# Optimization experiments

Hardware: AMD Instinct MI355X
Metric: run time of the kernel (lower is better)

The kernel has to match this reference:

```python
import jax, jax.numpy as jnp
import numpy as np
from jax import lax

SPATIAL_K = 30
FEATURE_K = 6
EPS = 1e-12  # F.normalize eps


def setup_inputs() -> dict:
    key = jax.random.key(0)
    k1, k2 = jax.random.split(key)
    N, D = 10000, 256
    ema_feat = jax.random.normal(k1, (N, D), dtype=jnp.float32)
    pos = jax.random.randint(k2, (N, 2), 0, 512, dtype=jnp.int64)
    return {"ema_feat": ema_feat, "pos": pos}


def _spatial_candidates(pos, k_spatial):
    # Brute-force k-NN on 2D integer positions (replaces sklearn KD-tree).
    posf = pos.astype(jnp.float32)  # [N, 2]
    sq = jnp.sum(posf * posf, axis=-1)  # [N]
    d2 = sq[:, None] + sq[None, :] - 2.0 * (posf @ posf.T)  # [N, N]
    N = pos.shape[0]
    # exclude self (sklearn returns self first, code drops column 0)
    d2 = d2 + jnp.where(jnp.eye(N, dtype=bool), jnp.inf, 0.0).astype(d2.dtype)
    _, idx = lax.top_k(-d2, k_spatial)  # nearest = largest negative distance
    return idx  # [N, k_spatial]


def reference(ema_feat, pos):
    N = ema_feat.shape[0]
    k_spatial = min(SPATIAL_K, N - 1)
    k_feat = min(FEATURE_K, k_spatial)

    spatial_candidates = _spatial_candidates(pos, k_spatial)  # [N, Ks]

    # F.normalize(ema_feat, dim=-1): x / max(||x||, eps)
    norm = jnp.linalg.norm(ema_feat, axis=-1, keepdims=True)
    feat_norm = ema_feat / jnp.maximum(norm, EPS)  # [N, D]

    cand_feat = feat_norm[spatial_candidates]  # [N, Ks, D]
    sim = jnp.einsum("nd,nkd->nk", feat_norm, cand_feat)  # cosine sim [N, Ks]

    topk_sim, topk_local_idx = lax.top_k(sim, k_feat)  # [N, Kf]
    topk_indices = jnp.take_along_axis(spatial_candidates, topk_local_idx, axis=1)
    topk_weights = jax.nn.softmax(topk_sim, axis=-1)
    return topk_indices, topk_weights
```

## Files before the change

### kernel.cpp

```cpp
#include <hip/hip_runtime.h>
#include <cstdint>
#include <cstddef>

#define FD    256
#define KS    30
#define KF    6
#define CSH   4
#define GW    32
#define NCELLS (GW*GW)
#define BCAP  40
#define OVCAP 128
#define KREG  8
#define SCAPW 96
#define MAXC  100
#define PIPE  5

#define WFENCE() __threadfence_block()

__global__ __launch_bounds__(1024) void zero_kernel(int* __restrict__ cellCnt,
                                                    int* __restrict__ ovfCnt) {
  cellCnt[threadIdx.x] = 0;
  if (threadIdx.x == 0) *ovfCnt = 0;
}

__global__ __launch_bounds__(256) void prep_bin_kernel(const float* __restrict__ x,
                                                       float* __restrict__ y,
                                                       const int2* __restrict__ pos,
                                                       int* __restrict__ cellCnt,
                                                       int2* __restrict__ bucket,
                                                       int* __restrict__ ovfCnt,
                                                       int2* __restrict__ ovf, int N) {
  const int j = blockIdx.x * 256 + threadIdx.x;
  if (j < N) {
    int2 p = pos[j];
    const int cell = (p.y >> CSH) * GW + (p.x >> CSH);
    const int s = atomicAdd(&cellCnt[cell], 1);
    const int2 e = make_int2(p.x | (p.y << 16), j);
    if (s < BCAP) bucket[cell * BCAP + s] = e;
    else { int o = atomicAdd(ovfCnt, 1); if (o < OVCAP) ovf[o] = e; }
  }
  const int row = blockIdx.x * 4 + (threadIdx.x >> 6);
  if (row >= N) return;
  const int lane = threadIdx.x & 63;
  float4 v = ((const float4*)(x + (size_t)row * FD))[lane];
  float ss = v.x * v.x + v.y * v.y + v.z * v.z + v.w * v.w;
#pragma unroll
  for (int o = 32; o; o >>= 1) ss += __shfl_down(ss, o);
  ss = __shfl(ss, 0);
  const float d = fmaxf(sqrtf(ss), 1e-12f);
  float4 o4;
  o4.x = v.x / d; o4.y = v.y / d; o4.z = v.z / d; o4.w = v.w / d;
  ((float4*)(y + (size_t)row * FD))[lane] = o4;
}

__global__ __launch_bounds__(256) void compact_kernel(const int* __restrict__ cellCnt,
                                                      const int2* __restrict__ bucket,
                                                      const int* __restrict__ ovfCnt,
                                                      const int2* __restrict__ ovf,
                                                      int* __restrict__ qorder, int N) {
  const int w = threadIdx.x >> 6, lane = threadIdx.x & 63;
  const int cell = blockIdx.x * 4 + w;
  const int4* cc4 = (const int4*)cellCnt;
  int start = 0, total = 0;
#pragma unroll
  for (int c = 0; c < 4; ++c) {
    int4 v = cc4[c * 64 + lane];
    int s0 = min(v.x, BCAP), s1 = min(v.y, BCAP), s2 = min(v.z, BCAP), s3 = min(v.w, BCAP);
    int s = s0 + s1 + s2 + s3;
    int incl = s;
#pragma unroll
    for (int o = 1; o < 64; o <<= 1) { int u = __shfl_up(incl, o); if (lane >= o) incl += u; }
    const int cid0 = (c * 64 + lane) * 4;
    if (cell >= cid0 && cell < cid0 + 4) {
      int p = total + (incl - s);
      if (cell - cid0 > 0) p += s0;
      if (cell - cid0 > 1) p += s1;
      if (cell - cid0 > 2) p += s2;
      start = p;
    }
    total += __shfl(incl, 63);
  }
  start = __shfl(start, (cell >> 2) & 63);
  const int cnt = min(cellCnt[cell], BCAP);
  for (int s = lane; s < cnt; s += 64)
    qorder[start + s] = bucket[cell * BCAP + s].y;
  if (cell == NCELLS - 1) {
    const int on = min(*ovfCnt, OVCAP);
    for (int o = lane; o < on; o += 64) qorder[total + o] = ovf[o].y;
  }
}

__global__ __launch_bounds__(256, 6) void graph_kernel(const int2* __restrict__ pos,
                                                       const int* __restrict__ cellCnt,
                                                       const int2* __restrict__ bucket,
                                                       const int* __restrict__ ovfCnt,
                                                       const int2* __restrict__ ovf,
                                                       const int* __restrict__ qorder,
                                                       const float* __restrict__ fn,
                                                       float* __restrict__ outI,
                                                       float* __restrict__ outW, int N) {
  __shared__ float qf[4][FD];
  __shared__ unsigned long long surv[4][SCAPW];
  __shared__ int pfx[4][MAXC + 1];
  __shared__ int cbase[4][MAXC];
  __shared__ int hist[4][64];
  __shared__ float sims[4][KS];
  __shared__ int selj[4][KS];
  __shared__ int wsel[4][KF];
  __shared__ int kd2[4];

  const int w = threadIdx.x >> 6, lane = threadIdx.x & 63;
  const int qi = blockIdx.x * 4 + w;
  if (qi >= N) return;
  const int i = qorder[qi];

  float* qfw = qf[w];
  unsigned long long* survw = surv[w];
  int* pfxw = pfx[w];
  int* basew = cbase[w];
  int* histw = hist[w];
  float* simsw = sims[w];
  int* seljw = selj[w];
  int* wselw = wsel[w];

  const int2 q = pos[i];
  const int qx = q.x, qy = q.y;
  const int cx = qx >> CSH, cy = qy >> CSH;
  const int ovfN = min(*ovfCnt, OVCAP);

  ((float4*)qfw)[lane] = ((const float4*)(fn + (size_t)i * FD))[lane];
  WFENCE();

  int R = 2;
  int sn = 0;
  for (;;) {
    const int W = 2 * R + 1;
    const int ns = min(W * W, MAXC);
    int run = 0;
    for (int cb = 0; cb < ns; cb += 64) {
      const int s = cb + lane;
      int cnt = 0, base = 0;
      if (s < ns) {
        int dy = s / W - R, dx = s % W - R;
        int yy = cy + dy, xx = cx + dx;
        if (yy >= 0 && yy < GW && xx >= 0 && xx < GW) {
          int cid = yy * GW + xx;
          cnt = min(cellCnt[cid], BCAP);
          base = cid * BCAP;
        }
      }
      int incl = cnt;
#pragma unroll
      for (int o = 1; o < 64; o <<= 1) { int u = __shfl_up(incl, o); if (lane >= o) incl += u; }
      if (s < ns) { pfxw[s] = run + incl - cnt; basew[s] = base; }
      run += __shfl(incl, 63);
    }
    if (lane == 0) pfxw[ns] = run;
    WFENCE();
    const int M = run;
    const int MM = min(M + ovfN, 64 * KREG);

    unsigned long long kreg[KREG];
#pragma unroll
    for (int s8 = 0; s8 < KREG; ++s8) {
      kreg[s8] = ~0ull;
      const int m = lane + 64 * s8;
      if (m < MM) {
        int2 e;
        if (m < M) {
          int c = 0;
#pragma unroll
          for (int st = 64; st; st >>= 1) { int nc = c + st; if (nc < ns && pfxw[nc] <= m) c = nc; }
          e = bucket[basew[c] + (m - pfxw[c])];
        } else {
          e = ovf[m - M];
        }
        const int j = e.y;
        if (j != i) {
          int x = e.x & 0xffff, y = e.x >> 16;
          int dx = qx - x, dy = qy - y;
          unsigned d2 = (unsigned)(dx * dx + dy * dy);
          kreg[s8] = (((unsigned long long)d2) << 16) | (unsigned)j;
        }
      }
    }

    histw[lane] = 0;
    WFENCE();
#pragma unroll
    for (int s8 = 0; s8 < KREG; ++s8)
      if (kreg[s8] != ~0ull)
        atomicAdd(&histw[min((int)(kreg[s8] >> 22), 63)], 1);
    WFENCE();
    int cum = histw[lane];
#pragma unroll
    for (int o = 1; o < 64; o <<= 1) { int u = __shfl_up(cum, o); if (lane >= o) cum += u; }
    const unsigned long long bal = __ballot(cum >= KS);
    unsigned long long Tk;
    if (bal == 0) Tk = 0x7fffffffull << 16;
    else {
      int bb = __ffsll((unsigned long long)bal) - 1;
      Tk = (bb == 63) ? (0x7fffffffull << 16) : (((unsigned long long)(bb + 1) << 6) << 16);
    }

    int sbase = 0;
#pragma unroll
    for (int s8 = 0; s8 < KREG; ++s8) {
      const bool p = kreg[s8] < Tk;
      const unsigned long long mask = __ballot(p);
      if (p) {
        int idx = sbase + __popcll(mask & ((1ull << lane) - 1));
        if (idx < SCAPW) survw[idx] = kreg[s8];
      }
      sbase += __popcll(mask);
    }
    sn = min(sbase, SCAPW);
    WFENCE();

    for (int p = lane; p < sn; p += 64) {
      const unsigned long long kp = survw[p];
      int r = 0;
      for (int s = 0; s < sn; ++s) r += (survw[s] < kp) ? 1 : 0;
      if (r < KS) seljw[r] = (int)(kp & 0xffffu);
      if (r == KS - 1) kd2[w] = (int)(kp >> 16);
    }
    WFENCE();

    bool done = false;
    if (sn >= KS) {
      const int kthd2 = kd2[w];
      int sg = 1 << 15;
      if (cx - R > 0)      sg = min(sg, qx - ((cx - R) << CSH));
      if (cx + R < GW - 1) sg = min(sg, (((cx + R) << CSH) + 15) - qx);
      if (cy - R > 0)      sg = min(sg, qy - ((cy - R) << CSH));
      if (cy + R < GW - 1) sg = min(sg, (((cy + R) << CSH) + 15) - qy);
      done = kthd2 < (sg + 1) * (sg + 1);
    }
    if (done) break;
    ++R;
  }

  const float4 q4v = ((const float4*)qfw)[lane];
  float4 fbuf[PIPE];
#pragma unroll
  for (int c = 0; c < PIPE; ++c)
    fbuf[c] = ((const float4*)(fn + (size_t)seljw[c] * FD))[lane];
#pragma unroll
  for (int c = 0; c < KS; ++c) {
    const float4 f = fbuf[c % PIPE];
    if (c + PIPE < KS)
      fbuf[c % PIPE] = ((const float4*)(fn + (size_t)seljw[c + PIPE] * FD))[lane];
    float d = f.x * q4v.x + f.y * q4v.y + f.z * q4v.z + f.w * q4v.w;
#pragma unroll
    for (int o = 32; o; o >>= 1) d += __shfl_down(d, o);
    if (lane == 0) simsw[c] = d;
  }
  WFENCE();

  if (lane < KS) {
    const float simv = simsw[lane];
    int r = 0;
    for (int s = 0; s < KS; ++s) {
      const float so = simsw[s];
      if (so > simv || (so == simv && s < lane)) ++r;
    }
    if (r < KF) wselw[r] = lane;
  }
  WFENCE();

  if (lane < KF) {
    const float m = simsw[wselw[0]];
    float sum = 0.f, my = 0.f;
#pragma unroll
    for (int r = 0; r < KF; ++r) {
      float e = expf(simsw[wselw[r]] - m);
      sum += e;
      if (r == lane) my = e;
    }
    outI[(size_t)i * KF + lane] = (float)seljw[wselw[lane]];
    outW[(size_t)i * KF + lane] = my / sum;
  }
}

extern "C" void kernel_launch(void* const* d_in, const int* in_sizes, int n_in,
                              void* d_out, int out_size, void* d_ws, size_t ws_size,
                              hipStream_t stream) {
  const float* feat = (const float*)d_in[0];
  const int2* pos = (const int2*)d_in[1];
  const int N = in_sizes[1] / 2;

  char* ws = (char*)d_ws;
  float* fn = (float*)ws;
  size_t off = (size_t)N * FD * sizeof(float);
  int* cellCnt = (int*)(ws + off);  off += NCELLS * sizeof(int);
  int* ovfCnt  = (int*)(ws + off);  off += 2 * sizeof(int);
  int2* bucket = (int2*)(ws + off); off += (size_t)NCELLS * BCAP * sizeof(int2);
  int2* ovf    = (int2*)(ws + off); off += OVCAP * sizeof(int2);
  int* qorder  = (int*)(ws + off);  off += (size_t)N * sizeof(int);

  float* out = (float*)d_out;

  zero_kernel<<<1, 1024, 0, stream>>>(cellCnt, ovfCnt);
  prep_bin_kernel<<<(N + 3) / 4, 256, 0, stream>>>(feat, fn, pos, cellCnt, bucket,
                                                   ovfCnt, ovf, N);
  compact_kernel<<<NCELLS / 4, 256, 0, stream>>>(cellCnt, bucket, ovfCnt, ovf, qorder, N);
  graph_kernel<<<(N + 3) / 4, 256, 0, stream>>>(pos, cellCnt, bucket, ovfCnt, ovf, qorder,
                                                fn, out, out + (size_t)N * KF, N);
}
```

Baseline: 111.7 us.

## Stage union of neighbor cell buckets in shared memory per block

The four queries in a block now compute the union of their R=2 cell windows. When that union is small enough, the block cooperatively loads all candidate bucket entries into shared memory once, and each wave's first radius iteration reads from there instead of doing per-wave prefix sums and global gathers. This adds block-wide __syncthreads and extra LDS usage, which may lower occupancy. The feature-gather prefetch depth is also doubled.

```diff
diff --git a/kernel.cpp b/kernel.cpp
--- a/kernel.cpp
+++ b/kernel.cpp
@@ -13,7 +13,9 @@
 #define KREG  8
 #define SCAPW 96
 #define MAXC  100
-#define PIPE  5
+#define PIPE  10
+#define SPCAP 512
+#define SNS   36
 
 #define WFENCE() __threadfence_block()
 
@@ -108,10 +110,16 @@
   __shared__ int selj[4][KS];
   __shared__ int wsel[4][KF];
   __shared__ int kd2[4];
+  __shared__ int2 spp[SPCAP];
+  __shared__ int spfx[SNS + 1];
+  __shared__ int sbase[SNS];
+  __shared__ int bcx[4], bcy[4];
+  __shared__ int sM;
 
   const int w = threadIdx.x >> 6, lane = threadIdx.x & 63;
-  const int qi = blockIdx.x * 4 + w;
-  if (qi >= N) return;
+  const int t = threadIdx.x;
+  const int qi0 = blockIdx.x * 4 + w;
+  const int qi = min(qi0, N - 1);
   const int i = qorder[qi];
 
   float* qfw = qf[w];
@@ -129,35 +137,77 @@
   const int ovfN = min(*ovfCnt, OVCAP);
 
   ((float4*)qfw)[lane] = ((const float4*)(fn + (size_t)i * FD))[lane];
-  WFENCE();
+  if (lane == 0) { bcx[w] = cx; bcy[w] = cy; }
+  __syncthreads();
+
+  const int ux0 = max(min(min(bcx[0], bcx[1]), min(bcx[2], bcx[3])) - 2, 0);
+  const int ux1 = min(max(max(bcx[0], bcx[1]), max(bcx[2], bcx[3])) + 2, GW - 1);
+  const int uy0 = max(min(min(bcy[0], bcy[1]), min(bcy[2], bcy[3])) - 2, 0);
+  const int uy1 = min(max(max(bcy[0], bcy[1]), max(bcy[2], bcy[3])) + 2, GW - 1);
+  const int uw = ux1 - ux0 + 1, uh = uy1 - uy0 + 1;
+  const int nsu = uw * uh;
+  const bool sharedOK = (nsu <= SNS);
+  int M_s = -1;
+  if (sharedOK) {
+    if (t < nsu) {
+      const int cid = (uy0 + t / uw) * GW + (ux0 + t % uw);
+      sbase[t] = cid * BCAP;
+      spfx[t] = min(cellCnt[cid], BCAP);
+    }
+    __syncthreads();
+    if (t == 0) {
+      int run = 0;
+      for (int c = 0; c < nsu; ++c) { int v = spfx[c]; spfx[c] = run; run += v; }
+      spfx[nsu] = run;
+      sM = (run <= SPCAP) ? run : -1;
+    }
+    __syncthreads();
+    M_s = sM;
+    if (M_s >= 0) {
+      for (int m = t; m < M_s; m += 256) {
+        int c = 0;
+#pragma unroll
+        for (int st = 32; st; st >>= 1) { int nc = c + st; if (nc < nsu && spfx[nc] <= m) c = nc; }
+        spp[m] = bucket[sbase[c] + (m - spfx[c])];
+      }
+    }
+    __syncthreads();
+  }
+  if (qi0 >= N) return;
 
   int R = 2;
   int sn = 0;
+  bool useStaged = (sharedOK && M_s >= 0);
   for (;;) {
-    const int W = 2 * R + 1;
-    const int ns = min(W * W, MAXC);
-    int run = 0;
-    for (int cb = 0; cb < ns; cb += 64) {
-      const int s = cb + lane;
-      int cnt = 0, base = 0;
-      if (s < ns) {
-        int dy = s / W - R, dx = s % W - R;
-        int yy = cy + dy, xx = cx + dx;
-        if (yy >= 0 && yy < GW && xx >= 0 && xx < GW) {
-          int cid = yy * GW + xx;
-          cnt = min(cellCnt[cid], BCAP);
-          base = cid * BCAP;
+    int M;
+    if (useStaged) {
+      M = M_s;
+    } else {
+      const int W = 2 * R + 1;
+      const int ns = min(W * W, MAXC);
+      int run = 0;
+      for (int cb = 0; cb < ns; cb += 64) {
+        const int s = cb + lane;
+        int cnt = 0, base = 0;
+        if (s < ns) {
+          int dy = s / W - R, dx = s % W - R;
+          int yy = cy + dy, xx = cx + dx;
+          if (yy >= 0 && yy < GW && xx >= 0 && xx < GW) {
+            int cid = yy * GW + xx;
+            cnt = min(cellCnt[cid], BCAP);
+            base = cid * BCAP;
+          }
         }
+        int incl = cnt;
+#pragma unroll
+        for (int o = 1; o < 64; o <<= 1) { int u = __shfl_up(incl, o); if (lane >= o) incl += u; }
+        if (s < ns) { pfxw[s] = run + incl - cnt; basew[s] = base; }
+        run += __shfl(incl, 63);
       }
-      int incl = cnt;
-#pragma unroll
-      for (int o = 1; o < 64; o <<= 1) { int u = __shfl_up(incl, o); if (lane >= o) incl += u; }
-      if (s < ns) { pfxw[s] = run + incl - cnt; basew[s] = base; }
-      run += __shfl(incl, 63);
-    }
-    if (lane == 0) pfxw[ns] = run;
-    WFENCE();
-    const int M = run;
+      if (lane == 0) pfxw[ns] = run;
+      WFENCE();
+      M = run;
+    }
     const int MM = min(M + ovfN, 64 * KREG);
 
     unsigned long long kreg[KREG];
@@ -168,10 +218,16 @@
       if (m < MM) {
         int2 e;
         if (m < M) {
-          int c = 0;
-#pragma unroll
-          for (int st = 64; st; st >>= 1) { int nc = c + st; if (nc < ns && pfxw[nc] <= m) c = nc; }
-          e = bucket[basew[c] + (m - pfxw[c])];
+          if (useStaged) {
+            e = spp[m];
+          } else {
+            const int W = 2 * R + 1;
+            const int ns = min(W * W, MAXC);
+            int c = 0;
+#pragma unroll
+            for (int st = 64; st; st >>= 1) { int nc = c + st; if (nc < ns && pfxw[nc] <= m) c = nc; }
+            e = bucket[basew[c] + (m - pfxw[c])];
+          }
         } else {
           e = ovf[m - M];
         }
@@ -203,18 +259,18 @@
       Tk = (bb == 63) ? (0x7fffffffull << 16) : (((unsigned long long)(bb + 1) << 6) << 16);
     }
 
-    int sbase = 0;
+    int sbase2 = 0;
 #pragma unroll
     for (int s8 = 0; s8 < KREG; ++s8) {
       const bool p = kreg[s8] < Tk;
       const unsigned long long mask = __ballot(p);
       if (p) {
-        int idx = sbase + __popcll(mask & ((1ull << lane) - 1));
+        int idx = sbase2 + __popcll(mask & ((1ull << lane) - 1));
         if (idx < SCAPW) survw[idx] = kreg[s8];
       }
-      sbase += __popcll(mask);
-    }
-    sn = min(sbase, SCAPW);
+      sbase2 += __popcll(mask);
+    }
+    sn = min(sbase2, SCAPW);
     WFENCE();
 
     for (int p = lane; p < sn; p += 64) {
@@ -238,6 +294,7 @@
     }
     if (done) break;
     ++R;
+    useStaged = false;
   }
 
   const float4 q4v = ((const float4*)qfw)[lane];
```

Result: slower. 115.9 us (+3.7%).
